# Kernel optimization log

Measured on AMD Instinct MI355X. Metric: run time of the kernel, lower is better.

Reference implementation:

```python
import jax, jax.numpy as jnp
import numpy as np

N, IN_DIM, OUT_DIM, E = 50000, 64, 64, 800000


def setup_inputs() -> dict:
    key = jax.random.key(0)
    k1, k2, k3, k4 = jax.random.split(key, 4)
    x = jax.random.normal(k1, (N, IN_DIM), dtype=jnp.float32)
    edge_index = jax.random.randint(k2, (2, E), 0, N, dtype=jnp.int64)
    # nn.Linear(in_dim, out_dim): weight [out, in], bias [out]
    bound = 1.0 / np.sqrt(IN_DIM)
    W = jax.random.uniform(k3, (OUT_DIM, IN_DIM), minval=-bound, maxval=bound, dtype=jnp.float32)
    b = jax.random.uniform(k4, (OUT_DIM,), minval=-bound, maxval=bound, dtype=jnp.float32)
    return {"x": x, "edge_index": edge_index, "W": W, "b": b}


def reference(x, edge_index, W, b):
    row, col = edge_index[0], edge_index[1]
    n = x.shape[0]
    # deg = bincount(row, minlength=N) + 1e-6, shape [N, 1]
    deg = jnp.zeros((n,), dtype=jnp.float32).at[row].add(1.0)[:, None] + 1e-6
    # agg[row] += x[col]  (gather + scatter-add)
    agg = jnp.zeros_like(x).at[row].add(x[col])
    agg = agg / deg
    return agg @ W.T + b
```

## Files before the change

kernel.cpp:

```cpp
#include <hip/hip_runtime.h>
#include <hip/hip_bf16.h>

#define N_NODES 50000
#define DIM 64
#define N_EDGES 800000
#define CAP 64
#define NTHR 256
#define GB_ROWS 32
#define NGB 1563
#define NPB (N_EDGES / NTHR)
#define TOTAL_BLOCKS (NGB + NPB)


static __device__ inline unsigned int f2bf(float f) {
    __hip_bfloat16 h = __float2bfloat16(f);
    return (unsigned int)*reinterpret_cast<unsigned short*>(&h);
}
static __device__ inline float bf_lo(unsigned int u) { return __uint_as_float(u << 16); }
static __device__ inline float bf_hi(unsigned int u) { return __uint_as_float(u & 0xffff0000u); }

__global__ __launch_bounds__(NTHR, 8) void place_gemm_kernel(
    const int* __restrict__ ei, const float* __restrict__ x,
    const float* __restrict__ W, int* __restrict__ count,
    int* csr, unsigned short* __restrict__ yb)
{
    __shared__ uint4  Wb[512];
    __shared__ float4 xs4[GB_ROWS * 16];

    int t = threadIdx.x;
    int b = blockIdx.x;

    if (b % 3 == 0) {
        int g  = b / 3;
        int R0 = g * GB_ROWS;
        const float4* x4 = (const float4*)x;
        for (int i = t; i < GB_ROWS * 16; i += NTHR) {
            int q = R0 * 16 + i;
            xs4[i] = (q < N_NODES * 16) ? x4[q] : make_float4(0.f, 0.f, 0.f, 0.f);
        }
        for (int m = t; m < 512; m += NTHR) {
            int o = m & 63, j8 = m >> 6;
            const float* wr = W + o * DIM + j8 * 8;
            uint4 uw;
            uw.x = f2bf(wr[0]) | (f2bf(wr[1]) << 16);
            uw.y = f2bf(wr[2]) | (f2bf(wr[3]) << 16);
            uw.z = f2bf(wr[4]) | (f2bf(wr[5]) << 16);
            uw.w = f2bf(wr[6]) | (f2bf(wr[7]) << 16);
            Wb[m] = uw;
        }
        __syncthreads();

        int w = t >> 6, l = t & 63;
#pragma unroll
        for (int i = 0; i < 8; i++) {
            int rl = w * 8 + i;
            int r  = R0 + rl;
            if (r < N_NODES) {
                float acc = 0.f;
#pragma unroll
                for (int j8 = 0; j8 < 8; j8++) {
                    uint4  wq = Wb[j8 * 64 + l];
                    float4 x0 = xs4[rl * 16 + 2 * j8];
                    float4 x1 = xs4[rl * 16 + 2 * j8 + 1];
                    acc += x0.x * bf_lo(wq.x) + x0.y * bf_hi(wq.x)
                         + x0.z * bf_lo(wq.y) + x0.w * bf_hi(wq.y)
                         + x1.x * bf_lo(wq.z) + x1.y * bf_hi(wq.z)
                         + x1.z * bf_lo(wq.w) + x1.w * bf_hi(wq.w);
                }
                yb[(size_t)r * DIM + l] = (unsigned short)f2bf(acc);
            }
        }
    } else {
        int p = (b / 3) * 2 + (b % 3 - 1);
        int e = p * NTHR + t;
        int row = ei[e], col = ei[N_EDGES + e];
        int pos = atomicAdd(&count[row], 1);
        if (pos < CAP) csr[row * CAP + pos] = col;
    }
}

__global__ __launch_bounds__(NTHR) void agg_kernel(
    const unsigned short* __restrict__ yb, const int* __restrict__ count,
    const int* csr, const float* __restrict__ bias, float* out)
{
    int t   = threadIdx.x;
    int w   = t >> 6;
    int l   = t & 63;
    int sub = l & 7;
    int grp = l >> 3;
    int r   = blockIdx.x * 4 + w;

    int deg = count[r];
    int dc  = deg < CAP ? deg : CAP;
    int myc = csr[(size_t)r * CAP + l];

    const uint4* ybq = (const uint4*)yb;
    float s[8];
#pragma unroll
    for (int q = 0; q < 8; q++) s[q] = 0.f;

    for (int jb = 0; jb < dc; jb += 8) {
        int  j     = jb + grp;
        int  c     = __shfl(myc, j);
        bool valid = j < dc;
        int  cs    = valid ? c : 0;
        uint4 v = ybq[(size_t)cs * 8 + sub];
        if (valid) {
            s[0] += bf_lo(v.x); s[1] += bf_hi(v.x);
            s[2] += bf_lo(v.y); s[3] += bf_hi(v.y);
            s[4] += bf_lo(v.z); s[5] += bf_hi(v.z);
            s[6] += bf_lo(v.w); s[7] += bf_hi(v.w);
        }
    }
#pragma unroll
    for (int q = 0; q < 8; q++) {
        s[q] += __shfl_xor(s[q], 8);
        s[q] += __shfl_xor(s[q], 16);
        s[q] += __shfl_xor(s[q], 32);
    }

    if (grp == 0) {
        float inv_d = 1.0f / ((float)deg + 1e-6f);
        float4 b0 = ((const float4*)bias)[2 * sub];
        float4 b1 = ((const float4*)bias)[2 * sub + 1];
        float4 o0 = make_float4(s[0] * inv_d + b0.x, s[1] * inv_d + b0.y,
                                s[2] * inv_d + b0.z, s[3] * inv_d + b0.w);
        float4 o1 = make_float4(s[4] * inv_d + b1.x, s[5] * inv_d + b1.y,
                                s[6] * inv_d + b1.z, s[7] * inv_d + b1.w);
        ((float4*)(out + (size_t)r * DIM))[2 * sub]     = o0;
        ((float4*)(out + (size_t)r * DIM))[2 * sub + 1] = o1;
    }
}

extern "C" void kernel_launch(void* const* d_in, const int* in_sizes, int n_in,
                              void* d_out, int out_size, void* d_ws, size_t ws_size,
                              hipStream_t stream) {
    const float* x    = (const float*)d_in[0];
    const int*   ei   = (const int*)d_in[1];
    const float* W    = (const float*)d_in[2];
    const float* bias = (const float*)d_in[3];
    float* out = (float*)d_out;

    int*            count = (int*)d_ws;
    unsigned short* yb    = (unsigned short*)((char*)d_ws + 262144);
    int*            csr   = (int*)d_out;

    hipMemsetAsync(count, 0, N_NODES * sizeof(int), stream);
    place_gemm_kernel<<<TOTAL_BLOCKS, NTHR, 0, stream>>>(ei, x, W, count, csr, yb);
    agg_kernel<<<N_NODES / 4, NTHR, 0, stream>>>(yb, count, csr, bias, out);
}
```

Baseline: 146.1 us.

## Partition nodes into per-XCD slices so CSR build and aggregation stay cache-local

```diff
diff --git a/kernel.cpp b/kernel.cpp
--- a/kernel.cpp
+++ b/kernel.cpp
@@ -7,9 +7,10 @@
 #define CAP 64
 #define NTHR 256
 #define GB_ROWS 32
-#define NGB 1563
-#define NPB (N_EDGES / NTHR)
-#define TOTAL_BLOCKS (NGB + NPB)
+#define SLICE 6250
+#define NGROUP 196
+#define TOTAL_BLOCKS (NGROUP * 24)
+#define CHUNK_EDGES 2048
 
 
 static __device__ inline unsigned int f2bf(float f) {
@@ -29,24 +30,25 @@
 
     int t = threadIdx.x;
     int b = blockIdx.x;
+    int m = b % 24;
 
-    if (b % 3 == 0) {
-        int g  = b / 3;
+    if (m < 8) {
+        int g  = (b / 24) * 8 + m;
         int R0 = g * GB_ROWS;
         const float4* x4 = (const float4*)x;
         for (int i = t; i < GB_ROWS * 16; i += NTHR) {
             int q = R0 * 16 + i;
             xs4[i] = (q < N_NODES * 16) ? x4[q] : make_float4(0.f, 0.f, 0.f, 0.f);
         }
-        for (int m = t; m < 512; m += NTHR) {
-            int o = m & 63, j8 = m >> 6;
+        for (int k = t; k < 512; k += NTHR) {
+            int o = k & 63, j8 = k >> 6;
             const float* wr = W + o * DIM + j8 * 8;
             uint4 uw;
             uw.x = f2bf(wr[0]) | (f2bf(wr[1]) << 16);
             uw.y = f2bf(wr[2]) | (f2bf(wr[3]) << 16);
             uw.z = f2bf(wr[4]) | (f2bf(wr[5]) << 16);
             uw.w = f2bf(wr[6]) | (f2bf(wr[7]) << 16);
-            Wb[m] = uw;
+            Wb[k] = uw;
         }
         __syncthreads();
 
@@ -71,11 +73,21 @@
             }
         }
     } else {
-        int p = (b / 3) * 2 + (b % 3 - 1);
-        int e = p * NTHR + t;
-        int row = ei[e], col = ei[N_EDGES + e];
-        int pos = atomicAdd(&count[row], 1);
-        if (pos < CAP) csr[row * CAP + pos] = col;
+        int s    = b & 7;
+        int q    = (b / 24) * 2 + ((m - 8) >> 3);
+        int base = q * CHUNK_EDGES;
+#pragma unroll
+        for (int k = 0; k < CHUNK_EDGES / NTHR; k++) {
+            int e = base + k * NTHR + t;
+            if (e < N_EDGES) {
+                int row = ei[e];
+                if (row / SLICE == s) {
+                    int col = ei[N_EDGES + e];
+                    int pos = atomicAdd(&count[row], 1);
+                    if (pos < CAP) csr[row * CAP + pos] = col;
+                }
+            }
+        }
     }
 }
 
@@ -88,7 +100,11 @@
     int l   = t & 63;
     int sub = l & 7;
     int grp = l >> 3;
-    int r   = blockIdx.x * 4 + w;
+    int sb  = blockIdx.x & 7;
+    int i   = blockIdx.x >> 3;
+    int rl  = i * 4 + w;
+    if (rl >= SLICE) return;
+    int r = sb * SLICE + rl;
 
     int deg = count[r];
     int dc  = deg < CAP ? deg : CAP;
@@ -147,5 +163,5 @@
 
     hipMemsetAsync(count, 0, N_NODES * sizeof(int), stream);
     place_gemm_kernel<<<TOTAL_BLOCKS, NTHR, 0, stream>>>(ei, x, W, count, csr, yb);
-    agg_kernel<<<N_NODES / 4, NTHR, 0, stream>>>(yb, count, csr, bias, out);
+    agg_kernel<<<8 * ((SLICE + 3) / 4 + ((SLICE % 4) ? 0 : 0)), NTHR, 0, stream>>>(yb, count, csr, bias, out);
 }
```

New measurement: 132.4 us. 1.1x faster.
